# Kernel optimization log

Hardware: AMD Instinct MI355X
Metric: run time of the kernel (lower is better)

The kernel has to match this reference:

```python
import jax, jax.numpy as jnp
import numpy as np

N_TOKENS = 2048
D_MODEL = 1024
D_FF = 4 * D_MODEL
N_EXPERTS = 8
TOP_K = 2


def setup_inputs() -> dict:
    key = jax.random.key(0)
    k_x, k_g, k_w1, k_w2 = jax.random.split(key, 4)
    x = jax.random.normal(k_x, (N_TOKENS, D_MODEL), dtype=jnp.float32)
    # torch Linear stores weight as [out_features, in_features]
    gate_w = jax.random.normal(k_g, (N_EXPERTS, D_MODEL), dtype=jnp.float32) * 0.02
    w1 = jax.random.normal(k_w1, (N_EXPERTS, D_FF, D_MODEL), dtype=jnp.float32) * 0.02
    w2 = jax.random.normal(k_w2, (N_EXPERTS, D_MODEL, D_FF), dtype=jnp.float32) * 0.02
    return {"x": x, "gate_w": gate_w, "w1": w1, "w2": w2}


def reference(x, gate_w, w1, w2):
    # Gating: top-2 logits, softmax over just the selected two logits
    logits = jnp.einsum("nd,ed->ne", x, gate_w)            # [N, E]
    top_vals, top_idx = jax.lax.top_k(logits, TOP_K)         # [N, 2]
    top_w = jax.nn.softmax(top_vals, axis=-1)                # [N, 2]

    # Combine weight per (token, expert): sum of gate weights where routed
    cw = jnp.sum(jax.nn.one_hot(top_idx, N_EXPERTS, dtype=x.dtype)
                 * top_w[..., None], axis=1)                 # [N, E]

    # Per-expert FFN, masked-combined (single-process path of the module)
    out = jnp.zeros_like(x)
    for e in range(N_EXPERTS):
        h = jax.nn.gelu(x @ w1[e].T, approximate=False)      # [N, 4d] (nn.GELU = exact erf)
        y = h @ w2[e].T                                      # [N, d]
        out = out + cw[:, e:e + 1] * y
    return out
```

## Files before the change

kernel.cpp:

```cpp
#include <hip/hip_runtime.h>
#include <hip/hip_bf16.h>

typedef short short8 __attribute__((ext_vector_type(8)));
typedef float f32x4 __attribute__((ext_vector_type(4)));

#define N_TOKENS 2048
#define D_MODEL 1024
#define D_FF 4096
#define N_EXPERTS 8
#define TOTAL_SLOTS (N_TOKENS * 2)
#define BK 32
#define SPLITK2 4
#define KC2 (D_FF / SPLITK2)

static __device__ __forceinline__ unsigned int f2u(float f) {
    union { float f; unsigned int u; } v; v.f = f; return v.u;
}

static __device__ __forceinline__ unsigned short f2bf(float f) {
    unsigned int u = f2u(f);
    unsigned int r = (u + 0x7fffu + ((u >> 16) & 1u)) >> 16;
    return (unsigned short)r;
}

static __device__ __forceinline__ unsigned int pk2bf(float a, float b) {
    __hip_bfloat162 t = __float22bfloat162_rn(float2{a, b});
    unsigned int u;
    __builtin_memcpy(&u, &t, 4);
    return u;
}

typedef __attribute__((address_space(1))) const unsigned int GU;
typedef __attribute__((address_space(3))) unsigned int LU;
static __device__ __forceinline__ void gload_lds16(const void* g, void* l) {
    __builtin_amdgcn_global_load_lds((GU*)g, (LU*)l, 16, 0, 0);
}

__global__ __launch_bounds__(256) void cvt_w_kernel(const float* __restrict__ src,
                                                    unsigned short* __restrict__ dst,
                                                    int n8) {
    int i = blockIdx.x * 256 + threadIdx.x;
    const int stride = gridDim.x * 256;
    for (; i < n8; i += stride) {
        const size_t b = (size_t)i * 8;
        float4 f0 = *(const float4*)(src + b);
        float4 f1 = *(const float4*)(src + b + 4);
        uint4 o;
        o.x = pk2bf(f0.x, f0.y); o.y = pk2bf(f0.z, f0.w);
        o.z = pk2bf(f1.x, f1.y); o.w = pk2bf(f1.z, f1.w);
        *(uint4*)(dst + b) = o;
    }
}

__global__ __launch_bounds__(256) void cvt_x_kernel(const float* __restrict__ x,
                                                    unsigned short* __restrict__ xb) {
    int i = (blockIdx.x * 256 + threadIdx.x) * 4;
    if (i >= N_TOKENS * D_MODEL) return;
    float4 f = *(const float4*)(x + i);
    uint2 o;
    o.x = pk2bf(f.x, f.y);
    o.y = pk2bf(f.z, f.w);
    *(uint2*)(xb + i) = o;
}

__global__ __launch_bounds__(64) void gate_kernel(const float* __restrict__ x,
                                                  const float* __restrict__ gw,
                                                  int* __restrict__ counts,
                                                  int* __restrict__ tok_e,
                                                  float* __restrict__ tok_w) {
    const int n = blockIdx.x;
    const int lane = threadIdx.x;
    float p[N_EXPERTS];
#pragma unroll
    for (int e = 0; e < N_EXPERTS; ++e) p[e] = 0.f;
    const float* xr = x + n * D_MODEL;
    for (int d = lane; d < D_MODEL; d += 64) {
        float xv = xr[d];
#pragma unroll
        for (int e = 0; e < N_EXPERTS; ++e) p[e] += xv * gw[e * D_MODEL + d];
    }
#pragma unroll
    for (int e = 0; e < N_EXPERTS; ++e) {
        float v = p[e];
        for (int o = 32; o > 0; o >>= 1) v += __shfl_down(v, o);
        p[e] = v;
    }
    if (lane == 0) {
        int b1 = 0; float v1 = p[0];
        for (int e = 1; e < N_EXPERTS; ++e) if (p[e] > v1) { v1 = p[e]; b1 = e; }
        int b2 = -1; float v2 = -1e30f;
        for (int e = 0; e < N_EXPERTS; ++e) if (e != b1 && p[e] > v2) { v2 = p[e]; b2 = e; }
        float e2 = __expf(v2 - v1);
        float s = 1.f + e2;
        tok_e[n * 2 + 0] = b1; tok_w[n * 2 + 0] = 1.f / s;
        tok_e[n * 2 + 1] = b2; tok_w[n * 2 + 1] = e2 / s;
        atomicAdd(&counts[b1], 1);
        atomicAdd(&counts[b2], 1);
    }
}

__global__ void scan_kernel(const int* __restrict__ counts,
                            int* __restrict__ offsets, int* __restrict__ fill) {
    if (threadIdx.x == 0 && blockIdx.x == 0) {
        int s = 0;
        for (int e = 0; e < N_EXPERTS; ++e) { offsets[e] = s; fill[e] = s; s += counts[e]; }
    }
}

__global__ __launch_bounds__(256) void route_kernel(const int* __restrict__ tok_e,
                                                    const float* __restrict__ tok_w,
                                                    int* __restrict__ fill,
                                                    int* __restrict__ rows_tok,
                                                    float* __restrict__ rows_w) {
    int i = blockIdx.x * 256 + threadIdx.x;
    if (i >= TOTAL_SLOTS) return;
    int e = tok_e[i];
    float w = tok_w[i];
    int pos = atomicAdd(&fill[e], 1);
    rows_tok[pos] = i >> 1;
    rows_w[pos] = w;
}

template <bool PRE>
__global__ __launch_bounds__(256, 4) void gemm1_kernel(
    const unsigned short* __restrict__ xb,
    const unsigned short* __restrict__ w1b,
    const float* __restrict__ w1f,
    const int* __restrict__ counts, const int* __restrict__ offsets,
    const int* __restrict__ rows_tok,
    unsigned short* __restrict__ h) {
    const int e = blockIdx.z;
    const int cnt = counts[e];
    const int mt = blockIdx.y;
    if (mt * 128 >= cnt) return;
    const int off = offsets[e];
    const int nt = blockIdx.x;

    __shared__ unsigned short As[2][128 * 32];
    __shared__ unsigned short Bs[2][128 * 32];

    const int tid = threadIdx.x, lane = tid & 63, wave = tid >> 6;
    const int wm = wave >> 1, wn = wave & 1;

    const int ac8 = lane & 3;
    int r0 = off + mt * 128 + wave * 32 + (lane >> 2);
    int r1 = r0 + 16;
    r0 = min(r0, TOTAL_SLOTS - 1);
    r1 = min(r1, TOTAL_SLOTS - 1);
    const unsigned short* ag0 = xb + (size_t)rows_tok[r0] * D_MODEL + ac8 * 8;
    const unsigned short* ag1 = xb + (size_t)rows_tok[r1] * D_MODEL + ac8 * 8;

    const int bgrow = nt * 128 + wave * 32 + (lane >> 2);
    const unsigned short* bg0 = w1b + (size_t)e * (D_FF * D_MODEL) + (size_t)bgrow * D_MODEL + ac8 * 8;
    const int brow = tid >> 1, bcol = (tid & 1) * 16;
    const float* bgf = w1f + (size_t)e * (D_FF * D_MODEL) + (size_t)(nt * 128 + brow) * D_MODEL + bcol;

    f32x4 acc[4][4];
#pragma unroll
    for (int i = 0; i < 4; ++i)
#pragma unroll
        for (int j = 0; j < 4; ++j) acc[i][j] = (f32x4){0.f, 0.f, 0.f, 0.f};

    auto stageA = [&](int buf, int t) {
        const int k = t * BK;
        gload_lds16(ag0 + k, &As[buf][(wave * 32) * 32]);
        gload_lds16(ag1 + k, &As[buf][(wave * 32 + 16) * 32]);
    };
    auto stageBpre = [&](int buf, int t) {
        const int k = t * BK;
        gload_lds16(bg0 + k, &Bs[buf][(wave * 32) * 32]);
        gload_lds16(bg0 + 16 * D_MODEL + k, &Bs[buf][(wave * 32 + 16) * 32]);
    };
    auto writeBf32 = [&](int buf, const float4& f0, const float4& f1,
                         const float4& f2, const float4& f3) {
        unsigned int bp[8];
        bp[0] = pk2bf(f0.x, f0.y); bp[1] = pk2bf(f0.z, f0.w);
        bp[2] = pk2bf(f1.x, f1.y); bp[3] = pk2bf(f1.z, f1.w);
        bp[4] = pk2bf(f2.x, f2.y); bp[5] = pk2bf(f2.z, f2.w);
        bp[6] = pk2bf(f3.x, f3.y); bp[7] = pk2bf(f3.z, f3.w);
        *(uint4*)&Bs[buf][brow * 32 + bcol]     = *(uint4*)&bp[0];
        *(uint4*)&Bs[buf][brow * 32 + bcol + 8] = *(uint4*)&bp[4];
    };

    stageA(0, 0);
    if constexpr (PRE) {
        stageBpre(0, 0);
    } else {
        float4 f0 = *(const float4*)(bgf + 0);
        float4 f1 = *(const float4*)(bgf + 4);
        float4 f2 = *(const float4*)(bgf + 8);
        float4 f3 = *(const float4*)(bgf + 12);
        writeBf32(0, f0, f1, f2, f3);
    }
    __syncthreads();

    const int KSTEPS = D_MODEL / BK;
#pragma unroll 2
    for (int t = 0; t < KSTEPS; ++t) {
        const int cur = t & 1, nxt = cur ^ 1;
        const bool more = (t + 1 < KSTEPS);
        float4 f0, f1, f2, f3;
        if (more) {
            stageA(nxt, t + 1);
            if constexpr (PRE) {
                stageBpre(nxt, t + 1);
            } else {
                const int k = (t + 1) * BK;
                f0 = *(const float4*)(bgf + k + 0);
                f1 = *(const float4*)(bgf + k + 4);
                f2 = *(const float4*)(bgf + k + 8);
                f3 = *(const float4*)(bgf + k + 12);
            }
        }
        short8 af[4], bfr[4];
#pragma unroll
        for (int mi = 0; mi < 4; ++mi)
            af[mi] = *(const short8*)&As[cur][(wm * 64 + mi * 16 + (lane & 15)) * 32 + (lane >> 4) * 8];
#pragma unroll
        for (int nj = 0; nj < 4; ++nj)
            bfr[nj] = *(const short8*)&Bs[cur][(wn * 64 + nj * 16 + (lane & 15)) * 32 + (lane >> 4) * 8];
#pragma unroll
        for (int mi = 0; mi < 4; ++mi)
#pragma unroll
            for (int nj = 0; nj < 4; ++nj)
                acc[mi][nj] = __builtin_amdgcn_mfma_f32_16x16x32_bf16(af[mi], bfr[nj], acc[mi][nj], 0, 0, 0);
        if constexpr (!PRE) {
            if (more) writeBf32(nxt, f0, f1, f2, f3);
        }
        __syncthreads();
    }

    const int lr = (lane >> 4) * 4, lc = lane & 15;
#pragma unroll
    for (int mi = 0; mi < 4; ++mi) {
        const int mbase = mt * 128 + wm * 64 + mi * 16 + lr;
#pragma unroll
        for (int j = 0; j < 4; ++j) {
            const int m = mbase + j;
            if (m < cnt) {
#pragma unroll
                for (int nj = 0; nj < 4; ++nj) {
                    const int n = nt * 128 + wn * 64 + nj * 16 + lc;
                    float v = acc[mi][nj][j];
                    v = 0.5f * v * (1.0f + erff(v * 0.70710678118654752f));
                    h[(size_t)(off + m) * D_FF + n] = f2bf(v);
                }
            }
        }
    }
}

template <bool PRE>
__global__ __launch_bounds__(256, 4) void gemm2_kernel(
    const unsigned short* __restrict__ h,
    const unsigned short* __restrict__ w2b,
    const float* __restrict__ w2f,
    const int* __restrict__ counts, const int* __restrict__ offsets,
    const int* __restrict__ rows_tok, const float* __restrict__ rows_w,
    float* __restrict__ out) {
    const int e = blockIdx.z >> 2;
    const int kc = blockIdx.z & 3;
    const int cnt = counts[e];
    const int mt = blockIdx.y;
    if (mt * 128 >= cnt) return;
    const int off = offsets[e];
    const int nt = blockIdx.x;

    __shared__ unsigned short As[2][128 * 32];
    __shared__ unsigned short Bs[2][128 * 32];

    const int tid = threadIdx.x, lane = tid & 63, wave = tid >> 6;
    const int wm = wave >> 1, wn = wave & 1;

    const int ac8 = lane & 3;
    int r0 = off + mt * 128 + wave * 32 + (lane >> 2);
    int r1 = r0 + 16;
    r0 = min(r0, TOTAL_SLOTS - 1);
    r1 = min(r1, TOTAL_SLOTS - 1);
    const unsigned short* ag0 = h + (size_t)r0 * D_FF + kc * KC2 + ac8 * 8;
    const unsigned short* ag1 = h + (size_t)r1 * D_FF + kc * KC2 + ac8 * 8;

    const int bgrow = nt * 128 + wave * 32 + (lane >> 2);
    const unsigned short* bg0 = w2b + (size_t)e * (D_MODEL * D_FF) + (size_t)bgrow * D_FF + kc * KC2 + ac8 * 8;
    const int brow = tid >> 1, bcol = (tid & 1) * 16;
    const float* bgf = w2f + (size_t)e * (D_MODEL * D_FF) + (size_t)(nt * 128 + brow) * D_FF + kc * KC2 + bcol;

    f32x4 acc[4][4];
#pragma unroll
    for (int i = 0; i < 4; ++i)
#pragma unroll
        for (int j = 0; j < 4; ++j) acc[i][j] = (f32x4){0.f, 0.f, 0.f, 0.f};

    auto stageA = [&](int buf, int t) {
        const int k = t * BK;
        gload_lds16(ag0 + k, &As[buf][(wave * 32) * 32]);
        gload_lds16(ag1 + k, &As[buf][(wave * 32 + 16) * 32]);
    };
    auto stageBpre = [&](int buf, int t) {
        const int k = t * BK;
        gload_lds16(bg0 + k, &Bs[buf][(wave * 32) * 32]);
        gload_lds16(bg0 + 16 * D_FF + k, &Bs[buf][(wave * 32 + 16) * 32]);
    };
    auto writeBf32 = [&](int buf, const float4& f0, const float4& f1,
                         const float4& f2, const float4& f3) {
        unsigned int bp[8];
        bp[0] = pk2bf(f0.x, f0.y); bp[1] = pk2bf(f0.z, f0.w);
        bp[2] = pk2bf(f1.x, f1.y); bp[3] = pk2bf(f1.z, f1.w);
        bp[4] = pk2bf(f2.x, f2.y); bp[5] = pk2bf(f2.z, f2.w);
        bp[6] = pk2bf(f3.x, f3.y); bp[7] = pk2bf(f3.z, f3.w);
        *(uint4*)&Bs[buf][brow * 32 + bcol]     = *(uint4*)&bp[0];
        *(uint4*)&Bs[buf][brow * 32 + bcol + 8] = *(uint4*)&bp[4];
    };

    stageA(0, 0);
    if constexpr (PRE) {
        stageBpre(0, 0);
    } else {
        float4 f0 = *(const float4*)(bgf + 0);
        float4 f1 = *(const float4*)(bgf + 4);
        float4 f2 = *(const float4*)(bgf + 8);
        float4 f3 = *(const float4*)(bgf + 12);
        writeBf32(0, f0, f1, f2, f3);
    }
    __syncthreads();

    const int KSTEPS = KC2 / BK;
#pragma unroll 2
    for (int t = 0; t < KSTEPS; ++t) {
        const int cur = t & 1, nxt = cur ^ 1;
        const bool more = (t + 1 < KSTEPS);
        float4 f0, f1, f2, f3;
        if (more) {
            stageA(nxt, t + 1);
            if constexpr (PRE) {
                stageBpre(nxt, t + 1);
            } else {
                const int k = (t + 1) * BK;
                f0 = *(const float4*)(bgf + k + 0);
                f1 = *(const float4*)(bgf + k + 4);
                f2 = *(const float4*)(bgf + k + 8);
                f3 = *(const float4*)(bgf + k + 12);
            }
        }
        short8 af[4], bfr[4];
#pragma unroll
        for (int mi = 0; mi < 4; ++mi)
            af[mi] = *(const short8*)&As[cur][(wm * 64 + mi * 16 + (lane & 15)) * 32 + (lane >> 4) * 8];
#pragma unroll
        for (int nj = 0; nj < 4; ++nj)
            bfr[nj] = *(const short8*)&Bs[cur][(wn * 64 + nj * 16 + (lane & 15)) * 32 + (lane >> 4) * 8];
#pragma unroll
        for (int mi = 0; mi < 4; ++mi)
#pragma unroll
            for (int nj = 0; nj < 4; ++nj)
                acc[mi][nj] = __builtin_amdgcn_mfma_f32_16x16x32_bf16(af[mi], bfr[nj], acc[mi][nj], 0, 0, 0);
        if constexpr (!PRE) {
            if (more) writeBf32(nxt, f0, f1, f2, f3);
        }
        __syncthreads();
    }

    const int lr = (lane >> 4) * 4, lc = lane & 15;
#pragma unroll
    for (int mi = 0; mi < 4; ++mi) {
        const int mbase = mt * 128 + wm * 64 + mi * 16 + lr;
#pragma unroll
        for (int j = 0; j < 4; ++j) {
            const int m = mbase + j;
            if (m < cnt) {
                const int tok = rows_tok[off + m];
                const float w = rows_w[off + m];
#pragma unroll
                for (int nj = 0; nj < 4; ++nj) {
                    const int n = nt * 128 + wn * 64 + nj * 16 + lc;
                    atomicAdd(&out[(size_t)tok * D_MODEL + n], w * acc[mi][nj][j]);
                }
            }
        }
    }
}


extern "C" void kernel_launch(void* const* d_in, const int* in_sizes, int n_in,
                              void* d_out, int out_size, void* d_ws, size_t ws_size,
                              hipStream_t stream) {
    const float* x  = (const float*)d_in[0];
    const float* gw = (const float*)d_in[1];
    const float* w1 = (const float*)d_in[2];
    const float* w2 = (const float*)d_in[3];
    float* out = (float*)d_out;

    char* ws = (char*)d_ws;
    int*   counts   = (int*)(ws + 0);
    int*   fill     = (int*)(ws + 256);
    int*   offsets  = (int*)(ws + 512);
    int*   tok_e    = (int*)(ws + 768);
    float* tok_w    = (float*)(ws + 17152);
    int*   rows_tok = (int*)(ws + 33536);
    float* rows_w   = (float*)(ws + 49920);
    unsigned short* xb  = (unsigned short*)(ws + 66560);
    unsigned short* h   = (unsigned short*)(ws + 4260864);
    unsigned short* w1b = (unsigned short*)(ws + 37815296ull);
    unsigned short* w2b = (unsigned short*)(ws + 104924160ull);
    const bool pre = (ws_size >= 172033024ull);

    hipMemsetAsync(counts, 0, 32, stream);
    hipMemsetAsync(d_out, 0, (size_t)out_size * sizeof(float), stream);

    if (pre) {
        const int n8 = (N_EXPERTS * D_FF * D_MODEL) / 8;
        cvt_w_kernel<<<dim3(2048), dim3(256), 0, stream>>>(w1, w1b, n8);
        cvt_w_kernel<<<dim3(2048), dim3(256), 0, stream>>>(w2, w2b, n8);
    }
    cvt_x_kernel<<<dim3((N_TOKENS * D_MODEL / 4 + 255) / 256), dim3(256), 0, stream>>>(x, xb);
    gate_kernel<<<dim3(N_TOKENS), dim3(64), 0, stream>>>(x, gw, counts, tok_e, tok_w);
    scan_kernel<<<dim3(1), dim3(64), 0, stream>>>(counts, offsets, fill);
    route_kernel<<<dim3((TOTAL_SLOTS + 255) / 256), dim3(256), 0, stream>>>(tok_e, tok_w, fill, rows_tok, rows_w);

    if (pre) {
        gemm1_kernel<true><<<dim3(D_FF / 128, 16, N_EXPERTS), dim3(256), 0, stream>>>(
            xb, w1b, w1, counts, offsets, rows_tok, h);
        gemm2_kernel<true><<<dim3(D_MODEL / 128, 16, N_EXPERTS * SPLITK2), dim3(256), 0, stream>>>(
            h, w2b, w2, counts, offsets, rows_tok, rows_w, out);
    } else {
        gemm1_kernel<false><<<dim3(D_FF / 128, 16, N_EXPERTS), dim3(256), 0, stream>>>(
            xb, w1b, w1, counts, offsets, rows_tok, h);
        gemm2_kernel<false><<<dim3(D_MODEL / 128, 16, N_EXPERTS * SPLITK2), dim3(256), 0, stream>>>(
            h, w2b, w2, counts, offsets, rows_tok, rows_w, out);
    }
}
```

Baseline: 345.5 us.

## Swizzle LDS tiles, remap blocks for XCD locality, drop fp32 weight fallback

Remaps the 1D grid so that all blocks sharing one (expert, M-tile) group land on the same XCD, which is meant to improve L2 reuse of the activation and weight tiles. An XOR swizzle is applied to the global-to-LDS column chunk and the matching LDS read offset, aiming to reduce LDS bank conflicts in the MFMA fragment loads. The fp32 on-the-fly weight conversion path is removed and pre-conversion always runs, which assumes the workspace is large enough.

```diff
diff --git a/kernel.cpp b/kernel.cpp
--- a/kernel.cpp
+++ b/kernel.cpp
@@ -121,20 +121,26 @@
     rows_w[pos] = w;
 }
 
-template <bool PRE>
+static __device__ __forceinline__ void xcd_decode(int b, int& g, int& member) {
+    const int xcd = b & 7;
+    const int s = b >> 3;
+    member = s & 31;
+    g = xcd + 8 * (s >> 5);
+}
+
+
 __global__ __launch_bounds__(256, 4) void gemm1_kernel(
     const unsigned short* __restrict__ xb,
     const unsigned short* __restrict__ w1b,
-    const float* __restrict__ w1f,
     const int* __restrict__ counts, const int* __restrict__ offsets,
     const int* __restrict__ rows_tok,
     unsigned short* __restrict__ h) {
-    const int e = blockIdx.z;
+    int g, member;
+    xcd_decode(blockIdx.x, g, member);
+    const int e = g >> 4, mt = g & 15, nt = member;
     const int cnt = counts[e];
-    const int mt = blockIdx.y;
     if (mt * 128 >= cnt) return;
     const int off = offsets[e];
-    const int nt = blockIdx.x;
 
     __shared__ unsigned short As[2][128 * 32];
     __shared__ unsigned short Bs[2][128 * 32];
@@ -142,18 +148,16 @@
     const int tid = threadIdx.x, lane = tid & 63, wave = tid >> 6;
     const int wm = wave >> 1, wn = wave & 1;
 
-    const int ac8 = lane & 3;
+    const int ss = (lane & 3) ^ ((lane >> 2) & 3);
     int r0 = off + mt * 128 + wave * 32 + (lane >> 2);
     int r1 = r0 + 16;
     r0 = min(r0, TOTAL_SLOTS - 1);
     r1 = min(r1, TOTAL_SLOTS - 1);
-    const unsigned short* ag0 = xb + (size_t)rows_tok[r0] * D_MODEL + ac8 * 8;
-    const unsigned short* ag1 = xb + (size_t)rows_tok[r1] * D_MODEL + ac8 * 8;
+    const unsigned short* ag0 = xb + (size_t)rows_tok[r0] * D_MODEL + ss * 8;
+    const unsigned short* ag1 = xb + (size_t)rows_tok[r1] * D_MODEL + ss * 8;
 
     const int bgrow = nt * 128 + wave * 32 + (lane >> 2);
-    const unsigned short* bg0 = w1b + (size_t)e * (D_FF * D_MODEL) + (size_t)bgrow * D_MODEL + ac8 * 8;
-    const int brow = tid >> 1, bcol = (tid & 1) * 16;
-    const float* bgf = w1f + (size_t)e * (D_FF * D_MODEL) + (size_t)(nt * 128 + brow) * D_MODEL + bcol;
+    const unsigned short* bg0 = w1b + (size_t)e * (D_FF * D_MODEL) + (size_t)bgrow * D_MODEL + ss * 8;
 
     f32x4 acc[4][4];
 #pragma unroll
@@ -161,72 +165,36 @@
 #pragma unroll
         for (int j = 0; j < 4; ++j) acc[i][j] = (f32x4){0.f, 0.f, 0.f, 0.f};
 
-    auto stageA = [&](int buf, int t) {
+    auto stage = [&](int buf, int t) {
         const int k = t * BK;
         gload_lds16(ag0 + k, &As[buf][(wave * 32) * 32]);
         gload_lds16(ag1 + k, &As[buf][(wave * 32 + 16) * 32]);
-    };
-    auto stageBpre = [&](int buf, int t) {
-        const int k = t * BK;
         gload_lds16(bg0 + k, &Bs[buf][(wave * 32) * 32]);
         gload_lds16(bg0 + 16 * D_MODEL + k, &Bs[buf][(wave * 32 + 16) * 32]);
     };
-    auto writeBf32 = [&](int buf, const float4& f0, const float4& f1,
-                         const float4& f2, const float4& f3) {
-        unsigned int bp[8];
-        bp[0] = pk2bf(f0.x, f0.y); bp[1] = pk2bf(f0.z, f0.w);
-        bp[2] = pk2bf(f1.x, f1.y); bp[3] = pk2bf(f1.z, f1.w);
-        bp[4] = pk2bf(f2.x, f2.y); bp[5] = pk2bf(f2.z, f2.w);
-        bp[6] = pk2bf(f3.x, f3.y); bp[7] = pk2bf(f3.z, f3.w);
-        *(uint4*)&Bs[buf][brow * 32 + bcol]     = *(uint4*)&bp[0];
-        *(uint4*)&Bs[buf][brow * 32 + bcol + 8] = *(uint4*)&bp[4];
-    };
-
-    stageA(0, 0);
-    if constexpr (PRE) {
-        stageBpre(0, 0);
-    } else {
-        float4 f0 = *(const float4*)(bgf + 0);
-        float4 f1 = *(const float4*)(bgf + 4);
-        float4 f2 = *(const float4*)(bgf + 8);
-        float4 f3 = *(const float4*)(bgf + 12);
-        writeBf32(0, f0, f1, f2, f3);
-    }
+
+    const int rsl = ((lane >> 4) ^ (lane & 3)) * 8;
+
+    stage(0, 0);
     __syncthreads();
 
     const int KSTEPS = D_MODEL / BK;
 #pragma unroll 2
     for (int t = 0; t < KSTEPS; ++t) {
-        const int cur = t & 1, nxt = cur ^ 1;
-        const bool more = (t + 1 < KSTEPS);
-        float4 f0, f1, f2, f3;
-        if (more) {
-            stageA(nxt, t + 1);
-            if constexpr (PRE) {
-                stageBpre(nxt, t + 1);
-            } else {
-                const int k = (t + 1) * BK;
-                f0 = *(const float4*)(bgf + k + 0);
-                f1 = *(const float4*)(bgf + k + 4);
-                f2 = *(const float4*)(bgf + k + 8);
-                f3 = *(const float4*)(bgf + k + 12);
-            }
-        }
+        const int cur = t & 1;
+        if (t + 1 < KSTEPS) stage(cur ^ 1, t + 1);
         short8 af[4], bfr[4];
 #pragma unroll
         for (int mi = 0; mi < 4; ++mi)
-            af[mi] = *(const short8*)&As[cur][(wm * 64 + mi * 16 + (lane & 15)) * 32 + (lane >> 4) * 8];
+            af[mi] = *(const short8*)&As[cur][(wm * 64 + mi * 16 + (lane & 15)) * 32 + rsl];
 #pragma unroll
         for (int nj = 0; nj < 4; ++nj)
-            bfr[nj] = *(const short8*)&Bs[cur][(wn * 64 + nj * 16 + (lane & 15)) * 32 + (lane >> 4) * 8];
+            bfr[nj] = *(const short8*)&Bs[cur][(wn * 64 + nj * 16 + (lane & 15)) * 32 + rsl];
 #pragma unroll
         for (int mi = 0; mi < 4; ++mi)
 #pragma unroll
             for (int nj = 0; nj < 4; ++nj)
                 acc[mi][nj] = __builtin_amdgcn_mfma_f32_16x16x32_bf16(af[mi], bfr[nj], acc[mi][nj], 0, 0, 0);
-        if constexpr (!PRE) {
-            if (more) writeBf32(nxt, f0, f1, f2, f3);
-        }
         __syncthreads();
     }
 
@@ -250,21 +218,19 @@
     }
 }
 
-template <bool PRE>
 __global__ __launch_bounds__(256, 4) void gemm2_kernel(
     const unsigned short* __restrict__ h,
     const unsigned short* __restrict__ w2b,
-    const float* __restrict__ w2f,
     const int* __restrict__ counts, const int* __restrict__ offsets,
     const int* __restrict__ rows_tok, const float* __restrict__ rows_w,
     float* __restrict__ out) {
-    const int e = blockIdx.z >> 2;
-    const int kc = blockIdx.z & 3;
+    int g, member;
+    xcd_decode(blockIdx.x, g, member);
+    const int e = g >> 4, mt = g & 15;
+    const int nt = member & 7, kc = member >> 3;
     const int cnt = counts[e];
-    const int mt = blockIdx.y;
     if (mt * 128 >= cnt) return;
     const int off = offsets[e];
-    const int nt = blockIdx.x;
 
     __shared__ unsigned short As[2][128 * 32];
     __shared__ unsigned short Bs[2][128 * 32];
@@ -272,18 +238,16 @@
     const int tid = threadIdx.x, lane = tid & 63, wave = tid >> 6;
     const int wm = wave >> 1, wn = wave & 1;
 
-    const int ac8 = lane & 3;
+    const int ss = (lane & 3) ^ ((lane >> 2) & 3);
     int r0 = off + mt * 128 + wave * 32 + (lane >> 2);
     int r1 = r0 + 16;
     r0 = min(r0, TOTAL_SLOTS - 1);
     r1 = min(r1, TOTAL_SLOTS - 1);
-    const unsigned short* ag0 = h + (size_t)r0 * D_FF + kc * KC2 + ac8 * 8;
-    const unsigned short* ag1 = h + (size_t)r1 * D_FF + kc * KC2 + ac8 * 8;
+    const unsigned short* ag0 = h + (size_t)r0 * D_FF + kc * KC2 + ss * 8;
+    const unsigned short* ag1 = h + (size_t)r1 * D_FF + kc * KC2 + ss * 8;
 
     const int bgrow = nt * 128 + wave * 32 + (lane >> 2);
-    const unsigned short* bg0 = w2b + (size_t)e * (D_MODEL * D_FF) + (size_t)bgrow * D_FF + kc * KC2 + ac8 * 8;
-    const int brow = tid >> 1, bcol = (tid & 1) * 16;
-    const float* bgf = w2f + (size_t)e * (D_MODEL * D_FF) + (size_t)(nt * 128 + brow) * D_FF + kc * KC2 + bcol;
+    const unsigned short* bg0 = w2b + (size_t)e * (D_MODEL * D_FF) + (size_t)bgrow * D_FF + kc * KC2 + ss * 8;
 
     f32x4 acc[4][4];
 #pragma unroll
@@ -291,72 +255,36 @@
 #pragma unroll
         for (int j = 0; j < 4; ++j) acc[i][j] = (f32x4){0.f, 0.f, 0.f, 0.f};
 
-    auto stageA = [&](int buf, int t) {
+    auto stage = [&](int buf, int t) {
         const int k = t * BK;
         gload_lds16(ag0 + k, &As[buf][(wave * 32) * 32]);
         gload_lds16(ag1 + k, &As[buf][(wave * 32 + 16) * 32]);
-    };
-    auto stageBpre = [&](int buf, int t) {
-        const int k = t * BK;
         gload_lds16(bg0 + k, &Bs[buf][(wave * 32) * 32]);
         gload_lds16(bg0 + 16 * D_FF + k, &Bs[buf][(wave * 32 + 16) * 32]);
     };
-    auto writeBf32 = [&](int buf, const float4& f0, const float4& f1,
-                         const float4& f2, const float4& f3) {
-        unsigned int bp[8];
-        bp[0] = pk2bf(f0.x, f0.y); bp[1] = pk2bf(f0.z, f0.w);
-        bp[2] = pk2bf(f1.x, f1.y); bp[3] = pk2bf(f1.z, f1.w);
-        bp[4] = pk2bf(f2.x, f2.y); bp[5] = pk2bf(f2.z, f2.w);
-        bp[6] = pk2bf(f3.x, f3.y); bp[7] = pk2bf(f3.z, f3.w);
-        *(uint4*)&Bs[buf][brow * 32 + bcol]     = *(uint4*)&bp[0];
-        *(uint4*)&Bs[buf][brow * 32 + bcol + 8] = *(uint4*)&bp[4];
-    };
-
-    stageA(0, 0);
-    if constexpr (PRE) {
-        stageBpre(0, 0);
-    } else {
-        float4 f0 = *(const float4*)(bgf + 0);
-        float4 f1 = *(const float4*)(bgf + 4);
-        float4 f2 = *(const float4*)(bgf + 8);
-        float4 f3 = *(const float4*)(bgf + 12);
-        writeBf32(0, f0, f1, f2, f3);
-    }
+
+    const int rsl = ((lane >> 4) ^ (lane & 3)) * 8;
+
+    stage(0, 0);
     __syncthreads();
 
     const int KSTEPS = KC2 / BK;
 #pragma unroll 2
     for (int t = 0; t < KSTEPS; ++t) {
-        const int cur = t & 1, nxt = cur ^ 1;
-        const bool more = (t + 1 < KSTEPS);
-        float4 f0, f1, f2, f3;
-        if (more) {
-            stageA(nxt, t + 1);
-            if constexpr (PRE) {
-                stageBpre(nxt, t + 1);
-            } else {
-                const int k = (t + 1) * BK;
-                f0 = *(const float4*)(bgf + k + 0);
-                f1 = *(const float4*)(bgf + k + 4);
-                f2 = *(const float4*)(bgf + k + 8);
-                f3 = *(const float4*)(bgf + k + 12);
-            }
-        }
+        const int cur = t & 1;
+        if (t + 1 < KSTEPS) stage(cur ^ 1, t + 1);
         short8 af[4], bfr[4];
 #pragma unroll
         for (int mi = 0; mi < 4; ++mi)
-            af[mi] = *(const short8*)&As[cur][(wm * 64 + mi * 16 + (lane & 15)) * 32 + (lane >> 4) * 8];
+            af[mi] = *(const short8*)&As[cur][(wm * 64 + mi * 16 + (lane & 15)) * 32 + rsl];
 #pragma unroll
         for (int nj = 0; nj < 4; ++nj)
-            bfr[nj] = *(const short8*)&Bs[cur][(wn * 64 + nj * 16 + (lane & 15)) * 32 + (lane >> 4) * 8];
+            bfr[nj] = *(const short8*)&Bs[cur][(wn * 64 + nj * 16 + (lane & 15)) * 32 + rsl];
 #pragma unroll
         for (int mi = 0; mi < 4; ++mi)
 #pragma unroll
             for (int nj = 0; nj < 4; ++nj)
                 acc[mi][nj] = __builtin_amdgcn_mfma_f32_16x16x32_bf16(af[mi], bfr[nj], acc[mi][nj], 0, 0, 0);
-        if constexpr (!PRE) {
-            if (more) writeBf32(nxt, f0, f1, f2, f3);
-        }
         __syncthreads();
     }
 
@@ -402,30 +330,18 @@
     unsigned short* h   = (unsigned short*)(ws + 4260864);
     unsigned short* w1b = (unsigned short*)(ws + 37815296ull);
     unsigned short* w2b = (unsigned short*)(ws + 104924160ull);
-    const bool pre = (ws_size >= 172033024ull);
 
     hipMemsetAsync(counts, 0, 32, stream);
     hipMemsetAsync(d_out, 0, (size_t)out_size * sizeof(float), stream);
 
-    if (pre) {
-        const int n8 = (N_EXPERTS * D_FF * D_MODEL) / 8;
-        cvt_w_kernel<<<dim3(2048), dim3(256), 0, stream>>>(w1, w1b, n8);
-        cvt_w_kernel<<<dim3(2048), dim3(256), 0, stream>>>(w2, w2b, n8);
-    }
+    const int n8 = (N_EXPERTS * D_FF * D_MODEL) / 8;
+    cvt_w_kernel<<<dim3(2048), dim3(256), 0, stream>>>(w1, w1b, n8);
+    cvt_w_kernel<<<dim3(2048), dim3(256), 0, stream>>>(w2, w2b, n8);
     cvt_x_kernel<<<dim3((N_TOKENS * D_MODEL / 4 + 255) / 256), dim3(256), 0, stream>>>(x, xb);
     gate_kernel<<<dim3(N_TOKENS), dim3(64), 0, stream>>>(x, gw, counts, tok_e, tok_w);
     scan_kernel<<<dim3(1), dim3(64), 0, stream>>>(counts, offsets, fill);
     route_kernel<<<dim3((TOTAL_SLOTS + 255) / 256), dim3(256), 0, stream>>>(tok_e, tok_w, fill, rows_tok, rows_w);
 
-    if (pre) {
-        gemm1_kernel<true><<<dim3(D_FF / 128, 16, N_EXPERTS), dim3(256), 0, stream>>>(
-            xb, w1b, w1, counts, offsets, rows_tok, h);
-        gemm2_kernel<true><<<dim3(D_MODEL / 128, 16, N_EXPERTS * SPLITK2), dim3(256), 0, stream>>>(
-            h, w2b, w2, counts, offsets, rows_tok, rows_w, out);
-    } else {
-        gemm1_kernel<false><<<dim3(D_FF / 128, 16, N_EXPERTS), dim3(256), 0, stream>>>(
-            xb, w1b, w1, counts, offsets, rows_tok, h);
-        gemm2_kernel<false><<<dim3(D_MODEL / 128, 16, N_EXPERTS * SPLITK2), dim3(256), 0, stream>>>(
-            h, w2b, w2, counts, offsets, rows_tok, rows_w, out);
-    }
-}
+    gemm1_kernel<<<dim3(4096), dim3(256), 0, stream>>>(xb, w1b, counts, offsets, rows_tok, h);
+    gemm2_kernel<<<dim3(4096), dim3(256), 0, stream>>>(h, w2b, counts, offsets, rows_tok, rows_w, out);
+}
```

Result: slower. 404.3 us (+17.0%).
